# Kernel tuning notes

Hardware: AMD Instinct MI355X
Metric: run time of the kernel (lower is better)

## Reference

```python
import jax, jax.numpy as jnp
import numpy as np

N_NODES = 5000
N_EDGES = 50000
HID = 64
OUT = 12
H, W = 12, 4
L = 3
BN_EPS = 1e-5
GEN_EPS = 1e-7


def setup_inputs() -> dict:
    key = jax.random.key(0)
    ks = jax.random.split(key, 12)
    node_feats = jax.random.normal(ks[0], (N_NODES, HID, H, W), dtype=jnp.float32)
    edge_feats = jax.random.normal(ks[1], (N_EDGES, HID, H, W), dtype=jnp.float32)
    src = jax.random.randint(ks[2], (N_EDGES,), 0, N_NODES)
    dst = jax.random.randint(ks[3], (N_EDGES,), 0, N_NODES)
    # per-layer params
    bn_gamma = jnp.ones((L, HID), dtype=jnp.float32)
    bn_beta = jnp.zeros((L, HID), dtype=jnp.float32)
    s = 1.0 / np.sqrt(HID)
    gen_W = jax.random.uniform(ks[4], (L, HID, HID), dtype=jnp.float32, minval=-s, maxval=s)
    gen_b = jax.random.uniform(ks[5], (L, HID), dtype=jnp.float32, minval=-s, maxval=s)
    out_W = jax.random.uniform(ks[6], (HID, OUT), dtype=jnp.float32, minval=-s, maxval=s)
    out_b = jax.random.uniform(ks[7], (OUT,), dtype=jnp.float32, minval=-s, maxval=s)
    return {
        "node_feats": node_feats, "edge_feats": edge_feats,
        "src": src, "dst": dst,
        "bn_gamma": bn_gamma, "bn_beta": bn_beta,
        "gen_W": gen_W, "gen_b": gen_b,
        "out_W": out_W, "out_b": out_b,
    }


def _batchnorm2d(x, gamma, beta):
    # training-mode BN over (N, H, W) per channel; x: [N, C, H, W]
    mu = jnp.mean(x, axis=(0, 2, 3), keepdims=True)
    var = jnp.mean((x - mu) ** 2, axis=(0, 2, 3), keepdims=True)
    xn = (x - mu) * jax.lax.rsqrt(var + BN_EPS)
    return xn * gamma[None, :, None, None] + beta[None, :, None, None]


def _genconv(h, he, src, dst, Wg, bg):
    # DeeperGCN GENConv with softmax aggregator (beta=1), mlp_layers=1.
    # h: [N, C, H, W], he: [E, C, H, W]
    m = jax.nn.relu(h[src] + he) + GEN_EPS                      # [E, C, H, W]
    mx = jax.ops.segment_max(m, dst, num_segments=N_NODES)      # [N, C, H, W]
    e = jnp.exp(m - mx[dst])
    s = jax.ops.segment_sum(e, dst, num_segments=N_NODES)
    a = e / s[dst]                                              # edge softmax per dst
    agg = jax.ops.segment_sum(a * m, dst, num_segments=N_NODES)
    feats = h + agg
    # linear over channel dim
    return jnp.einsum('nchw,co->nohw', feats, Wg) + bg[None, :, None, None]


def reference(node_feats, edge_feats, src, dst, bn_gamma, bn_beta, gen_W, gen_b, out_W, out_b):
    hv = node_feats
    he = edge_feats
    for l in range(L):
        hv1 = _batchnorm2d(hv, bn_gamma[l], bn_beta[l])
        hv1 = jax.nn.relu(hv1)  # dropout p=0.0 -> identity
        hv = _genconv(hv1, he, src, dst, gen_W[l], gen_b[l]) + hv
    # AvgPooling(g, hv.transpose(0,3)): mean over dim 0 of [W,C,H,N] == mean over W of hv
    h_g = jnp.mean(hv, axis=3, keepdims=True) * hv              # [N, C, H, W]
    out = jnp.einsum('nchw,co->nohw', h_g, out_W) + out_b[None, :, None, None]
    return out
```

## Files before the change

### kernel.cpp

```cpp
#include <hip/hip_runtime.h>
#include <float.h>

#define NN 5000
#define NE 50000
#define C 64
#define CHW4 768
#define SPLIT 25
#define NPS 200
#define MAXD 64

typedef float f32x4 __attribute__((ext_vector_type(4)));
typedef unsigned int u32x2 __attribute__((ext_vector_type(2)));

__device__ __forceinline__ unsigned int pack_bf16(float a, float b) {
  unsigned int ua = __float_as_uint(a), ub = __float_as_uint(b);
  ua = (ua + 0x7FFFu + ((ua >> 16) & 1u)) >> 16;
  ub = (ub + 0x7FFFu + ((ub >> 16) & 1u)) & 0xFFFF0000u;
  return ua | ub;
}
__device__ __forceinline__ float bf_lo(unsigned int u) { return __uint_as_float(u << 16); }
__device__ __forceinline__ float bf_hi(unsigned int u) { return __uint_as_float(u & 0xFFFF0000u); }

__global__ void hist_kernel(const int* __restrict__ dst, int* __restrict__ cnt) {
  int e = blockIdx.x * 256 + threadIdx.x;
  if (e < NE) atomicAdd(&cnt[dst[e]], 1);
}

__global__ void scan_kernel(const int* __restrict__ cnt, int* __restrict__ off, int* __restrict__ cur) {
  __shared__ int tsum[256];
  int t = threadIdx.x;
  constexpr int PER = 20;
  int base = t * PER;
  int vals[PER];
  int local = 0;
#pragma unroll
  for (int i = 0; i < PER; i++) {
    int idx = base + i;
    int v = (idx < NN) ? cnt[idx] : 0;
    vals[i] = local;
    local += v;
  }
  tsum[t] = local;
  __syncthreads();
  for (int o = 1; o < 256; o <<= 1) {
    int v = (t >= o) ? tsum[t - o] : 0;
    __syncthreads();
    tsum[t] += v;
    __syncthreads();
  }
  int excl = (t == 0) ? 0 : tsum[t - 1];
#pragma unroll
  for (int i = 0; i < PER; i++) {
    int idx = base + i;
    if (idx < NN) {
      int o2 = excl + vals[i];
      off[idx] = o2;
      cur[idx] = o2;
    }
  }
  if (t == 255) off[NN] = excl + local;
}

__global__ void scatter_kernel(const int* __restrict__ dst, const int* __restrict__ src,
                               int* __restrict__ cur, int* __restrict__ eids, int* __restrict__ srcs) {
  int e = blockIdx.x * 256 + threadIdx.x;
  if (e < NE) {
    int p = atomicAdd(&cur[dst[e]], 1);
    eids[p] = e;
    srcs[p] = src[e];
  }
}

__global__ void bn_stats_kernel(const float* __restrict__ hv, float* __restrict__ statsN) {
  int c = blockIdx.x / SPLIT, s = blockIdx.x % SPLIT;
  int n0 = s * NPS;
  const float4* hv4 = (const float4*)hv;
  float sum = 0.f, ss = 0.f;
  for (int i = threadIdx.x; i < NPS * 12; i += 256) {
    int n = n0 + i / 12, p = i % 12;
    float4 v = hv4[(size_t)n * CHW4 + c * 12 + p];
    sum += v.x + v.y + v.z + v.w;
    ss += v.x * v.x + v.y * v.y + v.z * v.z + v.w * v.w;
  }
  __shared__ float rs[256], rq[256];
  rs[threadIdx.x] = sum;
  rq[threadIdx.x] = ss;
  __syncthreads();
  for (int o = 128; o > 0; o >>= 1) {
    if (threadIdx.x < o) {
      rs[threadIdx.x] += rs[threadIdx.x + o];
      rq[threadIdx.x] += rq[threadIdx.x + o];
    }
    __syncthreads();
  }
  if (threadIdx.x == 0) {
    int r = blockIdx.x & 7;
    atomicAdd(&statsN[r * 128 + c], rs[0]);
    atomicAdd(&statsN[r * 128 + 64 + c], rq[0]);
  }
}

__global__ void finalize2_kernel(const float* __restrict__ statsN, const float* __restrict__ gamma,
                                 const float* __restrict__ beta, float* __restrict__ sc,
                                 float* __restrict__ sh) {
  int c = threadIdx.x;
  if (c < C) {
    float s = 0.f, q = 0.f;
#pragma unroll
    for (int r = 0; r < 8; r++) {
      s += statsN[r * 128 + c];
      q += statsN[r * 128 + 64 + c];
    }
    const float inv = 1.f / 240000.f;
    float mu = s * inv;
    float var = q * inv - mu * mu;
    float scale = gamma[c] * rsqrtf(var + 1e-5f);
    sc[c] = scale;
    sh[c] = beta[c] - mu * scale;
  }
}

__global__ __launch_bounds__(256) void h1_kernel(const float* __restrict__ hv,
                                                 const float* __restrict__ sc,
                                                 const float* __restrict__ sh,
                                                 u32x2* __restrict__ h1g) {
  int idx = blockIdx.x * 256 + threadIdx.x;
  int q = idx % CHW4;
  int c = q / 12;
  float s = sc[c], b = sh[c];
  float4 v = ((const float4*)hv)[idx];
  float x0 = fmaxf(v.x * s + b, 0.f);
  float x1 = fmaxf(v.y * s + b, 0.f);
  float x2 = fmaxf(v.z * s + b, 0.f);
  float x3 = fmaxf(v.w * s + b, 0.f);
  u32x2 o;
  o.x = pack_bf16(x0, x1);
  o.y = pack_bf16(x2, x3);
  h1g[idx] = o;
}

template <bool FIRST, bool LAST>
__global__ __launch_bounds__(256) void aggregate_kernel(
    const float* __restrict__ hv, const float* __restrict__ he,
    const u32x2* __restrict__ h1g, u32x2* __restrict__ heb,
    const int* __restrict__ srcs, const int* __restrict__ eids, const int* __restrict__ off,
    const float* __restrict__ Wg, const float* __restrict__ bg,
    const float* __restrict__ sc, const float* __restrict__ sh,
    float* __restrict__ hvNext, float* __restrict__ statsNext,
    const float* __restrict__ oW, const float* __restrict__ ob,
    float* __restrict__ out) {
  __shared__ float Wl[4096];
  __shared__ float fl[3072];
  __shared__ float scl[64], shl[64];
  __shared__ int sS[MAXD], sE[MAXD];
  __shared__ float bsum[64], bsq[64];

  int n = blockIdx.x, t = threadIdx.x;
  for (int i = t; i < 4096; i += 256) Wl[i] = Wg[i];
  if (t < 64) {
    scl[t] = sc[t];
    shl[t] = sh[t];
    bsum[t] = 0.f;
    bsq[t] = 0.f;
  }
  __syncthreads();

  const float4* hv4 = (const float4*)hv;
  const f32x4* heV = (const f32x4*)he;

  float h1[12];
#pragma unroll
  for (int j = 0; j < 3; j++) {
    int q = t + j * 256;
    int c = q / 12;
    float s = scl[c], b = shl[c];
    float4 v = hv4[(size_t)n * CHW4 + q];
    h1[4 * j + 0] = fmaxf(v.x * s + b, 0.f);
    h1[4 * j + 1] = fmaxf(v.y * s + b, 0.f);
    h1[4 * j + 2] = fmaxf(v.z * s + b, 0.f);
    h1[4 * j + 3] = fmaxf(v.w * s + b, 0.f);
  }

  float S[12], T[12];
#pragma unroll
  for (int i = 0; i < 12; i++) {
    S[i] = 0.f;
    T[i] = 0.f;
  }

  int e0 = off[n], d = off[n + 1] - e0;
  for (int base = 0; base < d; base += MAXD) {
    int cnt = min(MAXD, d - base);
    __syncthreads();
    if (t < cnt) {
      sS[t] = srcs[e0 + base + t];
      if (FIRST) sE[t] = eids[e0 + base + t];
    }
    __syncthreads();
#pragma unroll 2
    for (int k = 0; k < cnt; k++) {
      size_t hb = (size_t)sS[k] * CHW4;
      size_t pb = (size_t)(e0 + base + k) * CHW4;
#pragma unroll
      for (int j = 0; j < 3; j++) {
        int q = t + j * 256;
        u32x2 hg = h1g[hb + q];
        float hgf[4] = {bf_lo(hg.x), bf_hi(hg.x), bf_lo(hg.y), bf_hi(hg.y)};
        float hef[4];
        if (FIRST) {
          f32x4 b = __builtin_nontemporal_load(&heV[(size_t)sE[k] * CHW4 + q]);
          hef[0] = b.x; hef[1] = b.y; hef[2] = b.z; hef[3] = b.w;
          u32x2 o;
          o.x = pack_bf16(b.x, b.y);
          o.y = pack_bf16(b.z, b.w);
          __builtin_nontemporal_store(o, &heb[pb + q]);
        } else {
          u32x2 bb = __builtin_nontemporal_load(&heb[pb + q]);
          hef[0] = bf_lo(bb.x); hef[1] = bf_hi(bb.x); hef[2] = bf_lo(bb.y); hef[3] = bf_hi(bb.y);
        }
#pragma unroll
        for (int u = 0; u < 4; u++) {
          float m = fmaxf(hgf[u] + hef[u], 0.f) + 1e-7f;
          float e = __expf(m);
          int idx = j * 4 + u;
          S[idx] += e;
          T[idx] += e * m;
        }
      }
    }
  }

  bool hasE = d > 0;
  float4* fl4 = (float4*)fl;
#pragma unroll
  for (int j = 0; j < 3; j++) {
    int q = t + j * 256, idx = 4 * j;
    float4 f;
    f.x = h1[idx + 0] + (hasE ? T[idx + 0] / S[idx + 0] : 0.f);
    f.y = h1[idx + 1] + (hasE ? T[idx + 1] / S[idx + 1] : 0.f);
    f.z = h1[idx + 2] + (hasE ? T[idx + 2] / S[idx + 2] : 0.f);
    f.w = h1[idx + 3] + (hasE ? T[idx + 3] / S[idx + 3] : 0.f);
    fl4[q] = f;
  }
  __syncthreads();

  int o0 = (t / 12) * 4, hbp = t % 12;
  float4 acc[4];
  if (t < 192) {
#pragma unroll
    for (int i = 0; i < 4; i++) {
      float bv = bg[o0 + i];
      acc[i] = make_float4(bv, bv, bv, bv);
    }
    const float4* w4 = (const float4*)Wl;
    int widx = o0 >> 2;
    for (int c2 = 0; c2 < 64; c2++) {
      float4 fv = fl4[c2 * 12 + hbp];
      float4 wv = w4[c2 * 16 + widx];
      acc[0].x += wv.x * fv.x; acc[0].y += wv.x * fv.y; acc[0].z += wv.x * fv.z; acc[0].w += wv.x * fv.w;
      acc[1].x += wv.y * fv.x; acc[1].y += wv.y * fv.y; acc[1].z += wv.y * fv.z; acc[1].w += wv.y * fv.w;
      acc[2].x += wv.z * fv.x; acc[2].y += wv.z * fv.y; acc[2].z += wv.z * fv.z; acc[2].w += wv.z * fv.w;
      acc[3].x += wv.w * fv.x; acc[3].y += wv.w * fv.y; acc[3].z += wv.w * fv.z; acc[3].w += wv.w * fv.w;
    }
#pragma unroll
    for (int i = 0; i < 4; i++) {
      float4 r = hv4[(size_t)n * CHW4 + (o0 + i) * 12 + hbp];
      acc[i].x += r.x; acc[i].y += r.y; acc[i].z += r.z; acc[i].w += r.w;
    }
  }

  if constexpr (!LAST) {
    if (t < 192) {
      float4* hn4 = (float4*)hvNext;
#pragma unroll
      for (int i = 0; i < 4; i++) {
        hn4[(size_t)n * CHW4 + (o0 + i) * 12 + hbp] = acc[i];
        float s4 = acc[i].x + acc[i].y + acc[i].z + acc[i].w;
        float q4 = acc[i].x * acc[i].x + acc[i].y * acc[i].y + acc[i].z * acc[i].z + acc[i].w * acc[i].w;
        atomicAdd(&bsum[o0 + i], s4);
        atomicAdd(&bsq[o0 + i], q4);
      }
    }
    __syncthreads();
    int r = n & 7;
    if (t < 64) atomicAdd(&statsNext[r * 128 + t], bsum[t]);
    else if (t < 128) atomicAdd(&statsNext[r * 128 + 64 + (t - 64)], bsq[t - 64]);
  } else {
    __syncthreads();
    if (t < 192) {
#pragma unroll
      for (int i = 0; i < 4; i++) fl4[(o0 + i) * 12 + hbp] = acc[i];
    }
    for (int i = t; i < 768; i += 256) Wl[i] = oW[i];
    __syncthreads();
    for (int i = t; i < 768; i += 256) {
      float4 v = fl4[i];
      Wl[1024 + i] = (v.x + v.y + v.z + v.w) * 0.25f;
    }
    __syncthreads();
    if (t < 144) {
      int o = t / 12, hb = t % 12;
      float bias = ob[o];
      float4 a = make_float4(bias, bias, bias, bias);
      for (int c2 = 0; c2 < 64; c2++) {
        float4 v = fl4[c2 * 12 + hb];
        float wv = Wl[c2 * 12 + o] * Wl[1024 + c2 * 12 + hb];
        a.x += wv * v.x; a.y += wv * v.y; a.z += wv * v.z; a.w += wv * v.w;
      }
      ((float4*)out)[(size_t)n * 144 + t] = a;
    }
  }
}

extern "C" void kernel_launch(void* const* d_in, const int* in_sizes, int n_in,
                              void* d_out, int out_size, void* d_ws, size_t ws_size,
                              hipStream_t stream) {
  const float* node_feats = (const float*)d_in[0];
  const float* edge_feats = (const float*)d_in[1];
  const int* src = (const int*)d_in[2];
  const int* dst = (const int*)d_in[3];
  const float* bn_gamma = (const float*)d_in[4];
  const float* bn_beta = (const float*)d_in[5];
  const float* gen_W = (const float*)d_in[6];
  const float* gen_b = (const float*)d_in[7];
  const float* out_W = (const float*)d_in[8];
  const float* out_b = (const float*)d_in[9];
  float* out = (float*)d_out;

  char* ws = (char*)d_ws;
  float* hvA = (float*)ws;
  float* hvB = (float*)(ws + 61440000);
  u32x2* h1g = (u32x2*)(ws + 122880000);
  u32x2* heb = (u32x2*)(ws + 153600000);
  float* statsN = (float*)(ws + 460800000);
  float* sc = (float*)(ws + 460804096);
  float* sh = (float*)(ws + 460804352);
  int* cnt = (int*)(ws + 460804608);
  int* off = (int*)(ws + 460824608);
  int* cur = (int*)(ws + 460844612);
  int* eids = (int*)(ws + 460864612);
  int* srcs = (int*)(ws + 461064612);

  hipMemsetAsync(cnt, 0, NN * sizeof(int), stream);
  hist_kernel<<<(NE + 255) / 256, 256, 0, stream>>>(dst, cnt);
  scan_kernel<<<1, 256, 0, stream>>>(cnt, off, cur);
  scatter_kernel<<<(NE + 255) / 256, 256, 0, stream>>>(dst, src, cur, eids, srcs);

  hipMemsetAsync(statsN, 0, 1024 * sizeof(float), stream);
  bn_stats_kernel<<<C * SPLIT, 256, 0, stream>>>(node_feats, statsN);

  const float* hvPrev = node_feats;
  float* bufs[2] = {hvA, hvB};
  for (int l = 0; l < 3; l++) {
    finalize2_kernel<<<1, 64, 0, stream>>>(statsN, bn_gamma + l * C, bn_beta + l * C, sc, sh);
    h1_kernel<<<NN * CHW4 / 256, 256, 0, stream>>>(hvPrev, sc, sh, h1g);
    if (l == 0) {
      hipMemsetAsync(statsN, 0, 1024 * sizeof(float), stream);
      aggregate_kernel<true, false><<<NN, 256, 0, stream>>>(
          hvPrev, edge_feats, h1g, heb, srcs, eids, off, gen_W, gen_b,
          sc, sh, bufs[0], statsN, out_W, out_b, out);
      hvPrev = bufs[0];
    } else if (l == 1) {
      hipMemsetAsync(statsN, 0, 1024 * sizeof(float), stream);
      aggregate_kernel<false, false><<<NN, 256, 0, stream>>>(
          hvPrev, edge_feats, h1g, heb, srcs, eids, off, gen_W + C * C, gen_b + C,
          sc, sh, bufs[1], statsN, out_W, out_b, out);
      hvPrev = bufs[1];
    } else {
      aggregate_kernel<false, true><<<NN, 256, 0, stream>>>(
          hvPrev, edge_feats, h1g, heb, srcs, eids, off, gen_W + 2 * C * C, gen_b + 2 * C,
          sc, sh, bufs[0], statsN, out_W, out_b, out);
    }
  }
}
```

Before: 559.2 us.

## Fuse BN-apply into gather by storing raw bf16 hv from previous layer

```diff
diff --git a/kernel.cpp b/kernel.cpp
--- a/kernel.cpp
+++ b/kernel.cpp
@@ -5,12 +5,22 @@
 #define NE 50000
 #define C 64
 #define CHW4 768
-#define SPLIT 25
-#define NPS 200
 #define MAXD 64
 
 typedef float f32x4 __attribute__((ext_vector_type(4)));
 typedef unsigned int u32x2 __attribute__((ext_vector_type(2)));
+typedef unsigned int u32x4 __attribute__((ext_vector_type(4)));
+
+#if defined(__has_builtin)
+#if __has_builtin(__builtin_amdgcn_make_buffer_rsrc) && \
+    __has_builtin(__builtin_amdgcn_raw_buffer_load_b64) && \
+    __has_builtin(__builtin_amdgcn_raw_buffer_load_b128) && \
+    __has_builtin(__builtin_amdgcn_raw_buffer_store_b64)
+#define USE_BUF 1
+#endif
+#endif
+
+#define STREAM_AUX 19
 
 __device__ __forceinline__ unsigned int pack_bf16(float a, float b) {
   unsigned int ua = __float_as_uint(a), ub = __float_as_uint(b);
@@ -71,33 +81,33 @@
   }
 }
 
-__global__ void bn_stats_kernel(const float* __restrict__ hv, float* __restrict__ statsN) {
-  int c = blockIdx.x / SPLIT, s = blockIdx.x % SPLIT;
-  int n0 = s * NPS;
+__global__ __launch_bounds__(256) void init_kernel(const float* __restrict__ hv,
+                                                   u32x2* __restrict__ hvb,
+                                                   float* __restrict__ statsN) {
+  __shared__ float bsum[64], bsq[64];
+  int n = blockIdx.x, t = threadIdx.x;
+  if (t < 64) {
+    bsum[t] = 0.f;
+    bsq[t] = 0.f;
+  }
+  __syncthreads();
   const float4* hv4 = (const float4*)hv;
-  float sum = 0.f, ss = 0.f;
-  for (int i = threadIdx.x; i < NPS * 12; i += 256) {
-    int n = n0 + i / 12, p = i % 12;
-    float4 v = hv4[(size_t)n * CHW4 + c * 12 + p];
-    sum += v.x + v.y + v.z + v.w;
-    ss += v.x * v.x + v.y * v.y + v.z * v.z + v.w * v.w;
-  }
-  __shared__ float rs[256], rq[256];
-  rs[threadIdx.x] = sum;
-  rq[threadIdx.x] = ss;
-  __syncthreads();
-  for (int o = 128; o > 0; o >>= 1) {
-    if (threadIdx.x < o) {
-      rs[threadIdx.x] += rs[threadIdx.x + o];
-      rq[threadIdx.x] += rq[threadIdx.x + o];
-    }
-    __syncthreads();
-  }
-  if (threadIdx.x == 0) {
-    int r = blockIdx.x & 7;
-    atomicAdd(&statsN[r * 128 + c], rs[0]);
-    atomicAdd(&statsN[r * 128 + 64 + c], rq[0]);
-  }
+#pragma unroll
+  for (int j = 0; j < 3; j++) {
+    int q = t + j * 256;
+    int c = q / 12;
+    float4 v = hv4[(size_t)n * CHW4 + q];
+    u32x2 o;
+    o.x = pack_bf16(v.x, v.y);
+    o.y = pack_bf16(v.z, v.w);
+    hvb[(size_t)n * CHW4 + q] = o;
+    atomicAdd(&bsum[c], v.x + v.y + v.z + v.w);
+    atomicAdd(&bsq[c], v.x * v.x + v.y * v.y + v.z * v.z + v.w * v.w);
+  }
+  __syncthreads();
+  int r = n & 7;
+  if (t < 64) atomicAdd(&statsN[r * 128 + t], bsum[t]);
+  else if (t < 128) atomicAdd(&statsN[r * 128 + 64 + (t - 64)], bsq[t - 64]);
 }
 
 __global__ void finalize2_kernel(const float* __restrict__ statsN, const float* __restrict__ gamma,
@@ -120,29 +130,11 @@
   }
 }
 
-__global__ __launch_bounds__(256) void h1_kernel(const float* __restrict__ hv,
-                                                 const float* __restrict__ sc,
-                                                 const float* __restrict__ sh,
-                                                 u32x2* __restrict__ h1g) {
-  int idx = blockIdx.x * 256 + threadIdx.x;
-  int q = idx % CHW4;
-  int c = q / 12;
-  float s = sc[c], b = sh[c];
-  float4 v = ((const float4*)hv)[idx];
-  float x0 = fmaxf(v.x * s + b, 0.f);
-  float x1 = fmaxf(v.y * s + b, 0.f);
-  float x2 = fmaxf(v.z * s + b, 0.f);
-  float x3 = fmaxf(v.w * s + b, 0.f);
-  u32x2 o;
-  o.x = pack_bf16(x0, x1);
-  o.y = pack_bf16(x2, x3);
-  h1g[idx] = o;
-}
-
 template <bool FIRST, bool LAST>
 __global__ __launch_bounds__(256) void aggregate_kernel(
     const float* __restrict__ hv, const float* __restrict__ he,
-    const u32x2* __restrict__ h1g, u32x2* __restrict__ heb,
+    const u32x2* __restrict__ hvbIn, u32x2* __restrict__ hvbOut,
+    u32x2* __restrict__ heb,
     const int* __restrict__ srcs, const int* __restrict__ eids, const int* __restrict__ off,
     const float* __restrict__ Wg, const float* __restrict__ bg,
     const float* __restrict__ sc, const float* __restrict__ sh,
@@ -168,17 +160,23 @@
   const float4* hv4 = (const float4*)hv;
   const f32x4* heV = (const f32x4*)he;
 
-  float h1[12];
+#ifdef USE_BUF
+  auto srdHe = __builtin_amdgcn_make_buffer_rsrc((void*)he, (short)0, NE * 12288, 0x00020000);
+  auto srdHeb = __builtin_amdgcn_make_buffer_rsrc((void*)heb, (short)0, NE * 6144, 0x00020000);
+#endif
+
+  float scv[3], shv[3], h1[12];
 #pragma unroll
   for (int j = 0; j < 3; j++) {
     int q = t + j * 256;
     int c = q / 12;
-    float s = scl[c], b = shl[c];
+    scv[j] = scl[c];
+    shv[j] = shl[c];
     float4 v = hv4[(size_t)n * CHW4 + q];
-    h1[4 * j + 0] = fmaxf(v.x * s + b, 0.f);
-    h1[4 * j + 1] = fmaxf(v.y * s + b, 0.f);
-    h1[4 * j + 2] = fmaxf(v.z * s + b, 0.f);
-    h1[4 * j + 3] = fmaxf(v.w * s + b, 0.f);
+    h1[4 * j + 0] = fmaxf(v.x * scv[j] + shv[j], 0.f);
+    h1[4 * j + 1] = fmaxf(v.y * scv[j] + shv[j], 0.f);
+    h1[4 * j + 2] = fmaxf(v.z * scv[j] + shv[j], 0.f);
+    h1[4 * j + 3] = fmaxf(v.w * scv[j] + shv[j], 0.f);
   }
 
   float S[12], T[12];
@@ -200,22 +198,42 @@
 #pragma unroll 2
     for (int k = 0; k < cnt; k++) {
       size_t hb = (size_t)sS[k] * CHW4;
-      size_t pb = (size_t)(e0 + base + k) * CHW4;
+      int pbq = (e0 + base + k) * CHW4;
 #pragma unroll
       for (int j = 0; j < 3; j++) {
         int q = t + j * 256;
-        u32x2 hg = h1g[hb + q];
-        float hgf[4] = {bf_lo(hg.x), bf_hi(hg.x), bf_lo(hg.y), bf_hi(hg.y)};
+        u32x2 hg = hvbIn[hb + q];
+        float hgf[4];
+        hgf[0] = fmaxf(bf_lo(hg.x) * scv[j] + shv[j], 0.f);
+        hgf[1] = fmaxf(bf_hi(hg.x) * scv[j] + shv[j], 0.f);
+        hgf[2] = fmaxf(bf_lo(hg.y) * scv[j] + shv[j], 0.f);
+        hgf[3] = fmaxf(bf_hi(hg.y) * scv[j] + shv[j], 0.f);
         float hef[4];
         if (FIRST) {
-          f32x4 b = __builtin_nontemporal_load(&heV[(size_t)sE[k] * CHW4 + q]);
+          int ebq = sE[k] * CHW4 + q;
+          f32x4 b;
+#ifdef USE_BUF
+          u32x4 raw = __builtin_amdgcn_raw_buffer_load_b128(srdHe, ebq * 16, 0, STREAM_AUX);
+          b = __builtin_bit_cast(f32x4, raw);
+#else
+          b = __builtin_nontemporal_load(&heV[ebq]);
+#endif
           hef[0] = b.x; hef[1] = b.y; hef[2] = b.z; hef[3] = b.w;
           u32x2 o;
           o.x = pack_bf16(b.x, b.y);
           o.y = pack_bf16(b.z, b.w);
-          __builtin_nontemporal_store(o, &heb[pb + q]);
+#ifdef USE_BUF
+          __builtin_amdgcn_raw_buffer_store_b64(o, srdHeb, (pbq + q) * 8, 0, STREAM_AUX);
+#else
+          __builtin_nontemporal_store(o, &heb[pbq + q]);
+#endif
         } else {
-          u32x2 bb = __builtin_nontemporal_load(&heb[pb + q]);
+          u32x2 bb;
+#ifdef USE_BUF
+          bb = __builtin_amdgcn_raw_buffer_load_b64(srdHeb, (pbq + q) * 8, 0, STREAM_AUX);
+#else
+          bb = __builtin_nontemporal_load(&heb[pbq + q]);
+#endif
           hef[0] = bf_lo(bb.x); hef[1] = bf_hi(bb.x); hef[2] = bf_lo(bb.y); hef[3] = bf_hi(bb.y);
         }
 #pragma unroll
@@ -274,7 +292,12 @@
       float4* hn4 = (float4*)hvNext;
 #pragma unroll
       for (int i = 0; i < 4; i++) {
-        hn4[(size_t)n * CHW4 + (o0 + i) * 12 + hbp] = acc[i];
+        int pos = (o0 + i) * 12 + hbp;
+        hn4[(size_t)n * CHW4 + pos] = acc[i];
+        u32x2 ob2;
+        ob2.x = pack_bf16(acc[i].x, acc[i].y);
+        ob2.y = pack_bf16(acc[i].z, acc[i].w);
+        hvbOut[(size_t)n * CHW4 + pos] = ob2;
         float s4 = acc[i].x + acc[i].y + acc[i].z + acc[i].w;
         float q4 = acc[i].x * acc[i].x + acc[i].y * acc[i].y + acc[i].z * acc[i].z + acc[i].w * acc[i].w;
         atomicAdd(&bsum[o0 + i], s4);
@@ -330,16 +353,17 @@
   char* ws = (char*)d_ws;
   float* hvA = (float*)ws;
   float* hvB = (float*)(ws + 61440000);
-  u32x2* h1g = (u32x2*)(ws + 122880000);
-  u32x2* heb = (u32x2*)(ws + 153600000);
-  float* statsN = (float*)(ws + 460800000);
-  float* sc = (float*)(ws + 460804096);
-  float* sh = (float*)(ws + 460804352);
-  int* cnt = (int*)(ws + 460804608);
-  int* off = (int*)(ws + 460824608);
-  int* cur = (int*)(ws + 460844612);
-  int* eids = (int*)(ws + 460864612);
-  int* srcs = (int*)(ws + 461064612);
+  u32x2* hvbA = (u32x2*)(ws + 122880000);
+  u32x2* hvbB = (u32x2*)(ws + 153600000);
+  u32x2* heb = (u32x2*)(ws + 184320000);
+  float* statsN = (float*)(ws + 491520000);
+  float* sc = (float*)(ws + 491524096);
+  float* sh = (float*)(ws + 491524352);
+  int* cnt = (int*)(ws + 491524608);
+  int* off = (int*)(ws + 491544608);
+  int* cur = (int*)(ws + 491564612);
+  int* eids = (int*)(ws + 491584612);
+  int* srcs = (int*)(ws + 491784612);
 
   hipMemsetAsync(cnt, 0, NN * sizeof(int), stream);
   hist_kernel<<<(NE + 255) / 256, 256, 0, stream>>>(dst, cnt);
@@ -347,29 +371,22 @@
   scatter_kernel<<<(NE + 255) / 256, 256, 0, stream>>>(dst, src, cur, eids, srcs);
 
   hipMemsetAsync(statsN, 0, 1024 * sizeof(float), stream);
-  bn_stats_kernel<<<C * SPLIT, 256, 0, stream>>>(node_feats, statsN);
-
-  const float* hvPrev = node_feats;
-  float* bufs[2] = {hvA, hvB};
-  for (int l = 0; l < 3; l++) {
-    finalize2_kernel<<<1, 64, 0, stream>>>(statsN, bn_gamma + l * C, bn_beta + l * C, sc, sh);
-    h1_kernel<<<NN * CHW4 / 256, 256, 0, stream>>>(hvPrev, sc, sh, h1g);
-    if (l == 0) {
-      hipMemsetAsync(statsN, 0, 1024 * sizeof(float), stream);
-      aggregate_kernel<true, false><<<NN, 256, 0, stream>>>(
-          hvPrev, edge_feats, h1g, heb, srcs, eids, off, gen_W, gen_b,
-          sc, sh, bufs[0], statsN, out_W, out_b, out);
-      hvPrev = bufs[0];
-    } else if (l == 1) {
-      hipMemsetAsync(statsN, 0, 1024 * sizeof(float), stream);
-      aggregate_kernel<false, false><<<NN, 256, 0, stream>>>(
-          hvPrev, edge_feats, h1g, heb, srcs, eids, off, gen_W + C * C, gen_b + C,
-          sc, sh, bufs[1], statsN, out_W, out_b, out);
-      hvPrev = bufs[1];
-    } else {
-      aggregate_kernel<false, true><<<NN, 256, 0, stream>>>(
-          hvPrev, edge_feats, h1g, heb, srcs, eids, off, gen_W + 2 * C * C, gen_b + 2 * C,
-          sc, sh, bufs[0], statsN, out_W, out_b, out);
-    }
-  }
-}
+  init_kernel<<<NN, 256, 0, stream>>>(node_feats, hvbA, statsN);
+
+  finalize2_kernel<<<1, 64, 0, stream>>>(statsN, bn_gamma, bn_beta, sc, sh);
+  hipMemsetAsync(statsN, 0, 1024 * sizeof(float), stream);
+  aggregate_kernel<true, false><<<NN, 256, 0, stream>>>(
+      node_feats, edge_feats, hvbA, hvbB, heb, srcs, eids, off, gen_W, gen_b,
+      sc, sh, hvA, statsN, out_W, out_b, out);
+
+  finalize2_kernel<<<1, 64, 0, stream>>>(statsN, bn_gamma + C, bn_beta + C, sc, sh);
+  hipMemsetAsync(statsN, 0, 1024 * sizeof(float), stream);
+  aggregate_kernel<false, false><<<NN, 256, 0, stream>>>(
+      hvA, edge_feats, hvbB, hvbA, heb, srcs, eids, off, gen_W + C * C, gen_b + C,
+      sc, sh, hvB, statsN, out_W, out_b, out);
+
+  finalize2_kernel<<<1, 64, 0, stream>>>(statsN, bn_gamma + 2 * C, bn_beta + 2 * C, sc, sh);
+  aggregate_kernel<false, true><<<NN, 256, 0, stream>>>(
+      hvB, edge_feats, hvbA, hvbB, heb, srcs, eids, off, gen_W + 2 * C * C, gen_b + 2 * C,
+      sc, sh, hvA, statsN, out_W, out_b, out);
+}
```

After: 575.2 us. 2.9% more time.

## Fold BN finalize into consumers, merge memsets, and schedule nodes by descending degree

Applied to the files above, without the earlier changes.

```diff
diff --git a/kernel.cpp b/kernel.cpp
--- a/kernel.cpp
+++ b/kernel.cpp
@@ -21,13 +21,33 @@
 __device__ __forceinline__ float bf_lo(unsigned int u) { return __uint_as_float(u << 16); }
 __device__ __forceinline__ float bf_hi(unsigned int u) { return __uint_as_float(u & 0xFFFF0000u); }
 
+__device__ __forceinline__ void bn_finalize_block(const float* __restrict__ statsL,
+                                                  const float* __restrict__ gamma,
+                                                  const float* __restrict__ beta,
+                                                  int t, float* scl, float* shl) {
+  float s = 0.f, q = 0.f;
+#pragma unroll
+  for (int r = 0; r < 8; r++) {
+    s += statsL[r * 128 + t];
+    q += statsL[r * 128 + 64 + t];
+  }
+  const float inv = 1.f / 240000.f;
+  float mu = s * inv;
+  float var = q * inv - mu * mu;
+  float scale = gamma[t] * rsqrtf(var + 1e-5f);
+  scl[t] = scale;
+  shl[t] = beta[t] - mu * scale;
+}
+
 __global__ void hist_kernel(const int* __restrict__ dst, int* __restrict__ cnt) {
   int e = blockIdx.x * 256 + threadIdx.x;
   if (e < NE) atomicAdd(&cnt[dst[e]], 1);
 }
 
-__global__ void scan_kernel(const int* __restrict__ cnt, int* __restrict__ off, int* __restrict__ cur) {
+__global__ void scan_kernel(const int* __restrict__ cnt, int* __restrict__ off,
+                            int* __restrict__ cur, int* __restrict__ order) {
   __shared__ int tsum[256];
+  __shared__ int dh[64], dof[64];
   int t = threadIdx.x;
   constexpr int PER = 20;
   int base = t * PER;
@@ -59,6 +79,31 @@
     }
   }
   if (t == 255) off[NN] = excl + local;
+
+  if (t < 64) dh[t] = 0;
+  __syncthreads();
+  for (int idx = t; idx < NN; idx += 256) {
+    int deg = cnt[idx];
+    int b = deg > 63 ? 0 : 63 - deg;
+    atomicAdd(&dh[b], 1);
+  }
+  __syncthreads();
+  if (t == 0) {
+    int s = 0;
+    for (int i = 0; i < 64; i++) {
+      dof[i] = s;
+      s += dh[i];
+    }
+  }
+  __syncthreads();
+  if (t < 64) dh[t] = dof[t];
+  __syncthreads();
+  for (int idx = t; idx < NN; idx += 256) {
+    int deg = cnt[idx];
+    int b = deg > 63 ? 0 : 63 - deg;
+    int p = atomicAdd(&dh[b], 1);
+    order[p] = idx;
+  }
 }
 
 __global__ void scatter_kernel(const int* __restrict__ dst, const int* __restrict__ src,
@@ -100,34 +145,19 @@
   }
 }
 
-__global__ void finalize2_kernel(const float* __restrict__ statsN, const float* __restrict__ gamma,
-                                 const float* __restrict__ beta, float* __restrict__ sc,
-                                 float* __restrict__ sh) {
-  int c = threadIdx.x;
-  if (c < C) {
-    float s = 0.f, q = 0.f;
-#pragma unroll
-    for (int r = 0; r < 8; r++) {
-      s += statsN[r * 128 + c];
-      q += statsN[r * 128 + 64 + c];
-    }
-    const float inv = 1.f / 240000.f;
-    float mu = s * inv;
-    float var = q * inv - mu * mu;
-    float scale = gamma[c] * rsqrtf(var + 1e-5f);
-    sc[c] = scale;
-    sh[c] = beta[c] - mu * scale;
-  }
-}
-
 __global__ __launch_bounds__(256) void h1_kernel(const float* __restrict__ hv,
-                                                 const float* __restrict__ sc,
-                                                 const float* __restrict__ sh,
+                                                 const float* __restrict__ statsL,
+                                                 const float* __restrict__ gamma,
+                                                 const float* __restrict__ beta,
                                                  u32x2* __restrict__ h1g) {
-  int idx = blockIdx.x * 256 + threadIdx.x;
+  __shared__ float scl[64], shl[64];
+  int t = threadIdx.x;
+  if (t < 64) bn_finalize_block(statsL, gamma, beta, t, scl, shl);
+  __syncthreads();
+  int idx = blockIdx.x * 256 + t;
   int q = idx % CHW4;
   int c = q / 12;
-  float s = sc[c], b = sh[c];
+  float s = scl[c], b = shl[c];
   float4 v = ((const float4*)hv)[idx];
   float x0 = fmaxf(v.x * s + b, 0.f);
   float x1 = fmaxf(v.y * s + b, 0.f);
@@ -144,8 +174,10 @@
     const float* __restrict__ hv, const float* __restrict__ he,
     const u32x2* __restrict__ h1g, u32x2* __restrict__ heb,
     const int* __restrict__ srcs, const int* __restrict__ eids, const int* __restrict__ off,
+    const int* __restrict__ order,
     const float* __restrict__ Wg, const float* __restrict__ bg,
-    const float* __restrict__ sc, const float* __restrict__ sh,
+    const float* __restrict__ gamma, const float* __restrict__ beta,
+    const float* __restrict__ statsL,
     float* __restrict__ hvNext, float* __restrict__ statsNext,
     const float* __restrict__ oW, const float* __restrict__ ob,
     float* __restrict__ out) {
@@ -155,11 +187,10 @@
   __shared__ int sS[MAXD], sE[MAXD];
   __shared__ float bsum[64], bsq[64];
 
-  int n = blockIdx.x, t = threadIdx.x;
+  int n = order[blockIdx.x], t = threadIdx.x;
   for (int i = t; i < 4096; i += 256) Wl[i] = Wg[i];
   if (t < 64) {
-    scl[t] = sc[t];
-    shl[t] = sh[t];
+    bn_finalize_block(statsL, gamma, beta, t, scl, shl);
     bsum[t] = 0.f;
     bsq[t] = 0.f;
   }
@@ -200,7 +231,7 @@
 #pragma unroll 2
     for (int k = 0; k < cnt; k++) {
       size_t hb = (size_t)sS[k] * CHW4;
-      size_t pb = (size_t)(e0 + base + k) * CHW4;
+      size_t pbq = (size_t)(e0 + base + k) * CHW4;
 #pragma unroll
       for (int j = 0; j < 3; j++) {
         int q = t + j * 256;
@@ -213,9 +244,9 @@
           u32x2 o;
           o.x = pack_bf16(b.x, b.y);
           o.y = pack_bf16(b.z, b.w);
-          __builtin_nontemporal_store(o, &heb[pb + q]);
+          __builtin_nontemporal_store(o, &heb[pbq + q]);
         } else {
-          u32x2 bb = __builtin_nontemporal_load(&heb[pb + q]);
+          u32x2 bb = __builtin_nontemporal_load(&heb[pbq + q]);
           hef[0] = bf_lo(bb.x); hef[1] = bf_hi(bb.x); hef[2] = bf_lo(bb.y); hef[3] = bf_hi(bb.y);
         }
 #pragma unroll
@@ -333,43 +364,34 @@
   u32x2* h1g = (u32x2*)(ws + 122880000);
   u32x2* heb = (u32x2*)(ws + 153600000);
   float* statsN = (float*)(ws + 460800000);
-  float* sc = (float*)(ws + 460804096);
-  float* sh = (float*)(ws + 460804352);
-  int* cnt = (int*)(ws + 460804608);
-  int* off = (int*)(ws + 460824608);
-  int* cur = (int*)(ws + 460844612);
-  int* eids = (int*)(ws + 460864612);
-  int* srcs = (int*)(ws + 461064612);
-
-  hipMemsetAsync(cnt, 0, NN * sizeof(int), stream);
+  int* cnt = (int*)(ws + 460812288);
+  int* off = (int*)(ws + 460832288);
+  int* cur = (int*)(ws + 460852292);
+  int* eids = (int*)(ws + 460872292);
+  int* srcs = (int*)(ws + 461072292);
+  int* order = (int*)(ws + 461272292);
+
+  hipMemsetAsync(statsN, 0, 12288 + 20000, stream);
   hist_kernel<<<(NE + 255) / 256, 256, 0, stream>>>(dst, cnt);
-  scan_kernel<<<1, 256, 0, stream>>>(cnt, off, cur);
+  scan_kernel<<<1, 256, 0, stream>>>(cnt, off, cur, order);
   scatter_kernel<<<(NE + 255) / 256, 256, 0, stream>>>(dst, src, cur, eids, srcs);
-
-  hipMemsetAsync(statsN, 0, 1024 * sizeof(float), stream);
   bn_stats_kernel<<<C * SPLIT, 256, 0, stream>>>(node_feats, statsN);
 
-  const float* hvPrev = node_feats;
-  float* bufs[2] = {hvA, hvB};
-  for (int l = 0; l < 3; l++) {
-    finalize2_kernel<<<1, 64, 0, stream>>>(statsN, bn_gamma + l * C, bn_beta + l * C, sc, sh);
-    h1_kernel<<<NN * CHW4 / 256, 256, 0, stream>>>(hvPrev, sc, sh, h1g);
-    if (l == 0) {
-      hipMemsetAsync(statsN, 0, 1024 * sizeof(float), stream);
-      aggregate_kernel<true, false><<<NN, 256, 0, stream>>>(
-          hvPrev, edge_feats, h1g, heb, srcs, eids, off, gen_W, gen_b,
-          sc, sh, bufs[0], statsN, out_W, out_b, out);
-      hvPrev = bufs[0];
-    } else if (l == 1) {
-      hipMemsetAsync(statsN, 0, 1024 * sizeof(float), stream);
-      aggregate_kernel<false, false><<<NN, 256, 0, stream>>>(
-          hvPrev, edge_feats, h1g, heb, srcs, eids, off, gen_W + C * C, gen_b + C,
-          sc, sh, bufs[1], statsN, out_W, out_b, out);
-      hvPrev = bufs[1];
-    } else {
-      aggregate_kernel<false, true><<<NN, 256, 0, stream>>>(
-          hvPrev, edge_feats, h1g, heb, srcs, eids, off, gen_W + 2 * C * C, gen_b + 2 * C,
-          sc, sh, bufs[0], statsN, out_W, out_b, out);
-    }
-  }
-}
+  h1_kernel<<<NN * CHW4 / 256, 256, 0, stream>>>(node_feats, statsN, bn_gamma, bn_beta, h1g);
+  aggregate_kernel<true, false><<<NN, 256, 0, stream>>>(
+      node_feats, edge_feats, h1g, heb, srcs, eids, off, order,
+      gen_W, gen_b, bn_gamma, bn_beta, statsN,
+      hvA, statsN + 1024, out_W, out_b, out);
+
+  h1_kernel<<<NN * CHW4 / 256, 256, 0, stream>>>(hvA, statsN + 1024, bn_gamma + C, bn_beta + C, h1g);
+  aggregate_kernel<false, false><<<NN, 256, 0, stream>>>(
+      hvA, edge_feats, h1g, heb, srcs, eids, off, order,
+      gen_W + C * C, gen_b + C, bn_gamma + C, bn_beta + C, statsN + 1024,
+      hvB, statsN + 2048, out_W, out_b, out);
+
+  h1_kernel<<<NN * CHW4 / 256, 256, 0, stream>>>(hvB, statsN + 2048, bn_gamma + 2 * C, bn_beta + 2 * C, h1g);
+  aggregate_kernel<false, true><<<NN, 256, 0, stream>>>(
+      hvB, edge_feats, h1g, heb, srcs, eids, off, order,
+      gen_W + 2 * C * C, gen_b + 2 * C, bn_gamma + 2 * C, bn_beta + 2 * C, statsN + 2048,
+      hvA, statsN, out_W, out_b, out);
+}
```

Result: no change. 562.6 us (+0.6%).
